# Kernel optimization log

Measured on AMD Instinct MI355X. Metric: run time of the kernel, lower is better.

Reference implementation:

```python
import jax, jax.numpy as jnp
import numpy as np

N, C, K, KEIG, B, NG, H = 32768, 128, 5, 128, 64, 512, 4
E = 524288
EPS = 1e-5


def setup_inputs() -> dict:
    key = jax.random.key(0)
    ks = iter(jax.random.split(key, 40))
    def nrm(shape, scale):
        return jax.random.normal(next(ks), shape, jnp.float32) * scale
    s = 1.0 / np.sqrt(C)
    return dict(
        x=nrm((N, C), 1.0),
        U=nrm((N, KEIG), 1.0 / np.sqrt(N)),
        Lambda=jax.random.uniform(next(ks), (KEIG,), jnp.float32, 0.0, 2.0),
        lambda_max=jnp.full((1,), 2.0, jnp.float32),
        w_spa1=nrm((C, C), s), b_spa1=jnp.zeros((C,), jnp.float32),
        w_spa2=nrm((C, C), s), b_spa2=jnp.zeros((C,), jnp.float32),
        w_spe1=nrm((C, C), s), b_spe1=jnp.zeros((C,), jnp.float32),
        w_spe2=nrm((C, C), s), b_spe2=jnp.zeros((C,), jnp.float32),
        cheb_w=nrm((K, C, C), s), cheb_b=jnp.zeros((C,), jnp.float32),
        gamma=jnp.ones((1,), jnp.float32),
        w_proj=nrm((C, C), s),
        w_qkv=nrm((C, 3 * C), s), b_qkv=jnp.zeros((3 * C,), jnp.float32),
        w_out=nrm((C, C), s), b_out=jnp.zeros((C,), jnp.float32),
        mlp_w1=nrm((C, 2 * C), s), mlp_b1=jnp.zeros((2 * C,), jnp.float32),
        mlp_w2=nrm((2 * C, C), 1.0 / np.sqrt(2 * C)), mlp_b2=jnp.zeros((C,), jnp.float32),
        bn1_w=jnp.ones((C,), jnp.float32), bn1_b=jnp.zeros((C,), jnp.float32),
        bn2_w=jnp.ones((C,), jnp.float32), bn2_b=jnp.zeros((C,), jnp.float32),
        bn3_w=jnp.ones((C,), jnp.float32), bn3_b=jnp.zeros((C,), jnp.float32),
        edge_index=jax.random.randint(next(ks), (2, E), 0, N, jnp.int64) if jax.config.jax_enable_x64 else jax.random.randint(next(ks), (2, E), 0, N, jnp.int32),
        batch=jnp.repeat(jnp.arange(B), NG),  # 64 graphs of 512 nodes each
    )


def _mlp2(h, w1, b1, w2, b2):
    return jnp.maximum(h @ w1 + b1, 0.0) @ w2 + b2


def _bn(h, w, b):
    # train-mode BatchNorm1d over node dim (biased variance), GPSConv default norm
    mu = h.mean(0)
    var = jnp.mean((h - mu) ** 2, 0)
    return (h - mu) * jax.lax.rsqrt(var + EPS) * w + b


def _cheb(x, src, dst, lam, Ws, bias):
    # L_hat = (2/lambda_max) * (I - D^{-1/2} A D^{-1/2}) - I ; sym normalization
    deg = jax.ops.segment_sum(jnp.ones_like(src, x.dtype), src, num_segments=N)
    dis = jnp.where(deg > 0, 1.0 / jnp.sqrt(deg), 0.0)
    w = dis[src] * dis[dst]  # [E]
    scale = 2.0 / lam
    def lhat(v):
        agg = jax.ops.segment_sum(w[:, None] * v[src], dst, num_segments=N)
        return (scale - 1.0) * v - scale * agg
    Tx0 = x
    out = Tx0 @ Ws[0]
    Tx1 = lhat(Tx0)
    out = out + Tx1 @ Ws[1]
    for k in range(2, K):
        Tx2 = 2.0 * lhat(Tx1) - Tx0
        out = out + Tx2 @ Ws[k]
        Tx0, Tx1 = Tx1, Tx2
    return out + bias


def _mha(xd, w_qkv, b_qkv, w_out, b_out):
    Bq, n, _ = xd.shape
    dh = C // H
    qkv = xd @ w_qkv + b_qkv  # [B,n,3C]
    q, k, v = jnp.split(qkv, 3, axis=-1)
    heads = lambda t: t.reshape(Bq, n, H, dh).transpose(0, 2, 1, 3)
    q, k, v = heads(q), heads(k), heads(v)
    a = jax.nn.softmax(jnp.einsum('bhqd,bhkd->bhqk', q, k) / np.sqrt(dh), axis=-1)
    o = jnp.einsum('bhqk,bhkd->bhqd', a, v).transpose(0, 2, 1, 3).reshape(Bq, n, C)
    return o @ w_out + b_out


def reference(x, U, Lambda, lambda_max,
              w_spa1, b_spa1, w_spa2, b_spa2,
              w_spe1, b_spe1, w_spe2, b_spe2,
              cheb_w, cheb_b, gamma, w_proj,
              w_qkv, b_qkv, w_out, b_out,
              mlp_w1, mlp_b1, mlp_w2, mlp_b2,
              bn1_w, bn1_b, bn2_w, bn2_b, bn3_w, bn3_b,
              edge_index, batch):
    src, dst = edge_index[0], edge_index[1]
    lam = lambda_max[0]
    # ---- SpectralLocalNN (GPSConv local conv branch) ----
    x_sp = _mlp2(x, w_spa1, b_spa1, w_spa2, b_spa2)
    out_local = _cheb(x_sp, src, dst, lam, cheb_w, cheb_b)
    x_spec = _mlp2(x, w_spe1, b_spe1, w_spe2, b_spe2)
    h_proj = x_spec @ w_proj
    s_lam = jnp.exp(-gamma[0] * Lambda ** 2)  # [k_eig]
    out_spectral = U @ (s_lam[:, None] * (U.T @ h_proj))
    h1 = _bn(out_local + out_spectral + x, bn1_w, bn1_b)
    # ---- global attention branch (equal-size graphs -> dense reshape) ----
    xd = x.reshape(B, NG, C)
    h2 = _mha(xd, w_qkv, b_qkv, w_out, b_out).reshape(N, C)
    h2 = _bn(h2 + x, bn2_w, bn2_b)
    # ---- combine + MLP ----
    out = h1 + h2
    out = out + _mlp2(out, mlp_w1, mlp_b1, mlp_w2, mlp_b2)
    return _bn(out, bn3_w, bn3_b)
```

## Files before the change

### kernel.cpp

```cpp
#include <hip/hip_runtime.h>

typedef short bf16x8 __attribute__((ext_vector_type(8)));
typedef short bf16x4 __attribute__((ext_vector_type(4)));
typedef float f32x4 __attribute__((ext_vector_type(4)));

#define DEVI __device__ __forceinline__

constexpr int N   = 32768;
constexpr int C   = 128;
constexpr int E   = 524288;
constexpr float EPSV = 1e-5f;
constexpr int UT_BLOCKS = 256;
constexpr int HB  = 128;
constexpr int EPB = E / HB;
constexpr float QSCALE = 0.17677669529663687f * 1.4426950408889634f;

DEVI float bf2f(ushort u){ return __uint_as_float(((uint)u) << 16); }
DEVI ushort f2bf(float f){
  uint u = __float_as_uint(f);
  return (ushort)((u + 0x7fffu + ((u >> 16) & 1u)) >> 16);
}
DEVI uint cvtpk(float lo, float hi){
  uint r;
  asm("v_cvt_pk_bf16_f32 %0, %1, %2" : "=v"(r) : "v"(lo), "v"(hi));
  return r;
}
DEVI float fexp2(float x){
  float r;
  asm("v_exp_f32 %0, %1" : "=v"(r) : "v"(x));
  return r;
}
DEVI float sane(float v){ if (!(v == v)) return 0.f; return fminf(fmaxf(v, -1e30f), 1e30f); }
DEVI bool mode_fp32(const uint* lmraw){ return (lmraw[0] & 0xffffu) == 0u; }

constexpr int CSZ[28] = {128,1,16384,128,16384,128,16384,128,16384,128,81920,128,
                         1,16384,49152,384,16384,128,32768,256,32768,128,
                         128,128,128,128,128,128};
constexpr int COF[28] = {0,128,192,16576,16704,33088,33216,49600,49728,66112,
                         66240,148160,148288,148352,164736,213888,214272,230656,
                         230784,263552,263808,296576,296704,296832,296960,297088,
                         297216,297344};
constexpr int CAN_SMALL_TOTAL = 297472;

constexpr int WT_SPA1 = 0;
constexpr int WT_SPA2 = 16384;
constexpr int WT_SPE1 = 32768;
constexpr int WT_SPE2 = 49152;
constexpr int WT_PROJ = 65536;
constexpr int WT_CHEB = 81920;
constexpr int WT_QKV  = 163840;
constexpr int WT_WOUT = 212992;
constexpr int WT_MLP1 = 229376;
constexpr int WT_MLP2 = 262144;
constexpr int WT_TOTAL = 294912;

struct CvtArgs { const void* src[28]; };

DEVI ushort cvt_elem(const void* p, int j, bool f32){
  return f32 ? f2bf(((const float*)p)[j]) : ((const ushort*)p)[j];
}

__global__ __launch_bounds__(256) void prep_all(CvtArgs a,
    const void* __restrict__ xs, const void* __restrict__ Us,
    ushort* __restrict__ canx, ushort* __restrict__ canu,
    ushort* __restrict__ cs, ushort* __restrict__ wt,
    int* __restrict__ zp, const uint* __restrict__ lmraw)
{
  bool f32 = mode_fp32(lmraw);
  int b = blockIdx.x, tid = threadIdx.x;
  if (b < 8192) {
    size_t e = ((size_t)b * 256 + tid) * 4;
    bool isU = e >= (size_t)N * C;
    size_t off = isU ? e - (size_t)N * C : e;
    const void* src = isU ? Us : xs;
    ushort* dst = isU ? canu : canx;
    ushort4 o;
    if (f32) {
      float4 v = *(const float4*)((const float*)src + off);
      o.x = f2bf(v.x); o.y = f2bf(v.y); o.z = f2bf(v.z); o.w = f2bf(v.w);
    } else {
      o = *(const ushort4*)((const ushort*)src + off);
    }
    *(ushort4*)(dst + off) = o;
  } else if (b < 9354) {
    int idx = (b - 8192) * 256 + tid;
    #pragma unroll 1
    for (int s = 0; s < 28; s++) {
      if (idx < CSZ[s]) { cs[COF[s] + idx] = cvt_elem(a.src[s], idx, f32); return; }
      idx -= CSZ[s];
    }
  } else if (b < 10506) {
    int i = (b - 9354) * 256 + tid;
    if (i < 81920) {
      int m = i >> 14, r = i & 16383; int k = r >> 7, n = r & 127;
      const void* src = m==0?a.src[2] : m==1?a.src[4] : m==2?a.src[6] : m==3?a.src[8] : a.src[13];
      wt[m*16384 + n*128 + k] = cvt_elem(src, r, f32);
    } else if (i < 163840) {
      int j = i - 81920; int m = j >> 14, r = j & 16383; int k = r >> 7, n = r & 127;
      wt[WT_CHEB + n*640 + m*128 + k] = cvt_elem(a.src[10], j, f32);
    } else if (i < 212992) {
      int j = i - 163840; int k = j / 384, n = j % 384;
      wt[WT_QKV + n*128 + k] = cvt_elem(a.src[14], j, f32);
    } else if (i < 229376) {
      int j = i - 212992; int k = j >> 7, n = j & 127;
      wt[WT_WOUT + n*128 + k] = cvt_elem(a.src[16], j, f32);
    } else if (i < 262144) {
      int j = i - 229376; int k = j >> 8, n = j & 255;
      wt[WT_MLP1 + n*128 + k] = cvt_elem(a.src[18], j, f32);
    } else if (i < WT_TOTAL) {
      int j = i - 262144; int k = j >> 7, n = j & 127;
      wt[WT_MLP2 + n*256 + k] = cvt_elem(a.src[20], j, f32);
    }
  } else {
    int i = (b - 10506) * 256 + tid;
    if (i < 6144) zp[i] = 0;
  }
}

__global__ __launch_bounds__(1024) void hist_lds(const int* __restrict__ ei,
    int* __restrict__ cei, ushort* __restrict__ part)
{
  __shared__ uint hist[N / 2];
  int t = threadIdx.x;
  int b = blockIdx.x;
  bool i64 = ((ei[1] | ei[3] | ei[5] | ei[7]) == 0);
  size_t j0 = (size_t)b * EPB;
  #pragma unroll
  for (int i = t; i < N / 2; i += 1024) hist[i] = 0u;
  __syncthreads();
  for (int k = t; k < EPB; k += 1024) {
    size_t j = j0 + k;
    int v = (i64 ? ei[2 * j] : ei[j]) & (N - 1);
    cei[j] = v;
    atomicAdd(&hist[v >> 1], 1u << ((v & 1) * 16));
  }
  __syncthreads();
  uint* po = (uint*)(part + (size_t)b * N);
  for (int i = t; i < N / 2; i += 1024) po[i] = hist[i];
}

__global__ __launch_bounds__(256) void reduce_cnt(const ushort* __restrict__ part,
    int* __restrict__ cdt, float* __restrict__ dis)
{
  int d = blockIdx.x * 256 + threadIdx.x;
  int s = 0, tt = 0;
  #pragma unroll 8
  for (int b = 0; b < HB; b++) s  += part[(size_t)b * N + d];
  #pragma unroll 8
  for (int b = 0; b < HB; b++) tt += part[(size_t)(HB + b) * N + d];
  cdt[d] = tt;
  dis[d] = s > 0 ? rsqrtf((float)s) : 0.f;
}

__global__ __launch_bounds__(1024) void scan_kernel(const int* __restrict__ cnt,
                                                    int* __restrict__ row_ptr)
{
  __shared__ int sums[1024];
  int t = threadIdx.x;
  int loc[32]; int s = 0;
  int base = t * 32;
  #pragma unroll
  for (int i = 0; i < 32; i++) { loc[i] = s; s += cnt[base + i]; }
  sums[t] = s;
  __syncthreads();
  for (int off = 1; off < 1024; off <<= 1) {
    int v = (t >= off) ? sums[t - off] : 0;
    __syncthreads();
    sums[t] += v;
    __syncthreads();
  }
  int pre = (t == 0) ? 0 : sums[t - 1];
  #pragma unroll
  for (int i = 0; i < 32; i++) row_ptr[base + i] = pre + loc[i];
}

__global__ __launch_bounds__(256) void off_kernel(const int* __restrict__ rp,
    const ushort* __restrict__ part, int* __restrict__ off2)
{
  int d = blockIdx.x * 256 + threadIdx.x;
  int run = rp[d];
  #pragma unroll 8
  for (int b = 0; b < HB; b++) {
    off2[(size_t)b * N + d] = run;
    run += part[(size_t)(HB + b) * N + d];
  }
}

__global__ __launch_bounds__(1024) void edge_scatter(const int* __restrict__ cei,
    const int* __restrict__ off2, const float* __restrict__ dis,
    int2* __restrict__ ep)
{
  __shared__ int base[N];
  int t = threadIdx.x;
  int b = blockIdx.x;
  for (int i = t; i < N; i += 1024) base[i] = off2[(size_t)b * N + i];
  __syncthreads();
  size_t e0 = (size_t)b * EPB;
  for (int k = t; k < EPB; k += 1024) {
    size_t e = e0 + k;
    int s = cei[e], d = cei[e + E];
    int slot = atomicAdd(&base[d], 1);
    int2 v; v.x = s; v.y = __float_as_int(dis[s] * dis[d]);
    ep[slot] = v;
  }
}

template<int K, int COLS, bool RELU, int OMODE, bool BIAS, bool RES, int ASTR, int OSTR, bool QSC, bool STATS>
__global__ __launch_bounds__(256) void gemm_lds(
    const ushort* __restrict__ A, const ushort* __restrict__ WT,
    const ushort* __restrict__ bias, const ushort* __restrict__ res,
    void* __restrict__ outp, float* __restrict__ gstats)
{
  constexpr int NSEG = COLS / 128;
  constexpr int NKC = K / 128;
  constexpr int BP = 136;
  __shared__ ushort Bs[128 * BP];
  __shared__ float ls[STATS ? 256 : 1];
  int tid = threadIdx.x;
  int lane = tid & 63, wave = tid >> 6;
  int quad = lane >> 4, l16 = lane & 15;
  int seg = (NSEG > 1) ? (blockIdx.x % NSEG) : 0;
  int rb  = (NSEG > 1) ? (blockIdx.x / NSEG) : blockIdx.x;
  int row0 = rb * 64 + wave * 16;
  const ushort* wseg = WT + (size_t)(seg * 128) * K;

  f32x4 acc[8];
  #pragma unroll
  for (int nt = 0; nt < 8; nt++) acc[nt] = (f32x4){0.f, 0.f, 0.f, 0.f};

  for (int kc = 0; kc < NKC; kc++) {
    if (kc) __syncthreads();
    #pragma unroll
    for (int i = tid; i < 2048; i += 256) {
      int col = i >> 4, ko = (i & 15) * 8;
      *(bf16x8*)&Bs[col * BP + ko] =
          *(const bf16x8*)(wseg + (size_t)col * K + kc * 128 + ko);
    }
    __syncthreads();
    bf16x8 a[4];
    const ushort* ap = A + (size_t)(row0 + l16) * ASTR + kc * 128 + quad * 8;
    #pragma unroll
    for (int kk = 0; kk < 4; kk++) a[kk] = *(const bf16x8*)(ap + kk * 32);
    #pragma unroll
    for (int kk = 0; kk < 4; kk++) {
      #pragma unroll
      for (int nt = 0; nt < 8; nt++) {
        bf16x8 b = *(const bf16x8*)(&Bs[(nt * 16 + l16) * BP + kk * 32 + quad * 8]);
        acc[nt] = __builtin_amdgcn_mfma_f32_16x16x32_bf16(a[kk], b, acc[nt], 0, 0, 0);
      }
    }
  }

  if (STATS) {
    if (tid < 256) ls[tid] = 0.f;
    __syncthreads();
  }

  #pragma unroll
  for (int nt = 0; nt < 8; nt++) {
    int col = seg * 128 + nt * 16 + l16;
    float bv = 0.f;
    if (BIAS) bv = bf2f(bias[col]);
    float cs_ = 0.f, cs2 = 0.f;
    #pragma unroll
    for (int r = 0; r < 4; r++) {
      int row = row0 + quad * 4 + r;
      size_t oi = (size_t)row * OSTR + col;
      float v = acc[nt][r] + bv;
      if (RES) v += bf2f(res[(size_t)row * COLS + col]);
      if (RELU) v = fmaxf(v, 0.f);
      if (QSC && col < 128) v *= QSCALE;
      float nv;
      if (OMODE == 0)      { ((ushort*)outp)[oi] = f2bf(v); nv = v; }
      else if (OMODE == 1) { ((float*)outp)[oi] = v; nv = v; }
      else                 { float* fo = (float*)outp + oi; nv = *fo + v; *fo = nv; }
      if (STATS) { float sv = sane(nv); cs_ += sv; cs2 += sv * sv; }
    }
    if (STATS) { atomicAdd(&ls[col], cs_); atomicAdd(&ls[128 + col], cs2); }
  }

  if (STATS) {
    __syncthreads();
    float* gs = gstats + (blockIdx.x & 7) * 256;
    if (tid < 128) {
      atomicAdd(&gs[tid], ls[tid]);
      atomicAdd(&gs[128 + tid], ls[128 + tid]);
    }
  }
}

__global__ __launch_bounds__(256) void gemm_qkv(
    const ushort* __restrict__ A, const ushort* __restrict__ WT,
    const ushort* __restrict__ bias, ushort* __restrict__ outp)
{
  constexpr int BP = 136;
  __shared__ ushort Bs[128 * BP];
  int tid = threadIdx.x;
  int lane = tid & 63, wave = tid >> 6;
  int quad = lane >> 4, l16 = lane & 15;
  int row0 = blockIdx.x * 64 + wave * 16;
  bf16x8 a[4];
  {
    const ushort* ap = A + (size_t)(row0 + l16) * 128 + quad * 8;
    #pragma unroll
    for (int kk = 0; kk < 4; kk++) a[kk] = *(const bf16x8*)(ap + kk * 32);
  }

  #pragma unroll 1
  for (int seg = 0; seg < 3; seg++) {
    if (seg) __syncthreads();
    for (int i = tid; i < 2048; i += 256) {
      int col = i >> 4, ko = (i & 15) * 8;
      *(bf16x8*)&Bs[col * BP + ko] =
          *(const bf16x8*)(WT + (size_t)(seg * 128 + col) * 128 + ko);
    }
    __syncthreads();
    f32x4 acc[8];
    #pragma unroll
    for (int nt = 0; nt < 8; nt++) acc[nt] = (f32x4){0.f, 0.f, 0.f, 0.f};
    #pragma unroll
    for (int kk = 0; kk < 4; kk++)
      #pragma unroll
      for (int nt = 0; nt < 8; nt++) {
        bf16x8 b = *(const bf16x8*)(&Bs[(nt * 16 + l16) * BP + kk * 32 + quad * 8]);
        acc[nt] = __builtin_amdgcn_mfma_f32_16x16x32_bf16(a[kk], b, acc[nt], 0, 0, 0);
      }
    #pragma unroll
    for (int nt = 0; nt < 8; nt++) {
      int col = seg * 128 + nt * 16 + l16;
      float bv = bf2f(bias[col]);
      #pragma unroll
      for (int r = 0; r < 4; r++) {
        float v = acc[nt][r] + bv;
        if (seg == 0) v *= QSCALE;
        outp[(size_t)(row0 + quad * 4 + r) * 384 + col] = f2bf(v);
      }
    }
  }
}

template<bool THIRD, int OSTR>
__global__ __launch_bounds__(256) void gemm_chain(
    const ushort* __restrict__ A,
    const ushort* __restrict__ W1, const ushort* __restrict__ B1,
    const ushort* __restrict__ W2, const ushort* __restrict__ B2,
    const ushort* __restrict__ W3,
    ushort* __restrict__ outp)
{
  constexpr int BP = 136;
  __shared__ ushort Bs[128 * BP];
  __shared__ ushort Ts[64 * BP];
  int tid = threadIdx.x;
  int lane = tid & 63, wave = tid >> 6;
  int quad = lane >> 4, l16 = lane & 15;
  int row0 = blockIdx.x * 64 + wave * 16;
  int lw = wave * 16;

  for (int i = tid; i < 2048; i += 256) {
    int col = i >> 4, ko = (i & 15) * 8;
    *(bf16x8*)&Bs[col * BP + ko] = *(const bf16x8*)(W1 + (size_t)col * 128 + ko);
  }
  __syncthreads();
  bf16x8 a[4];
  {
    const ushort* ap = A + (size_t)(row0 + l16) * 128 + quad * 8;
    #pragma unroll
    for (int kk = 0; kk < 4; kk++) a[kk] = *(const bf16x8*)(ap + kk * 32);
  }
  f32x4 acc[8];
  #pragma unroll
  for (int nt = 0; nt < 8; nt++) acc[nt] = (f32x4){0.f, 0.f, 0.f, 0.f};
  #pragma unroll
  for (int kk = 0; kk < 4; kk++)
    #pragma unroll
    for (int nt = 0; nt < 8; nt++) {
      bf16x8 b = *(const bf16x8*)(&Bs[(nt * 16 + l16) * BP + kk * 32 + quad * 8]);
      acc[nt] = __builtin_amdgcn_mfma_f32_16x16x32_bf16(a[kk], b, acc[nt], 0, 0, 0);
    }
  #pragma unroll
  for (int nt = 0; nt < 8; nt++) {
    int col = nt * 16 + l16;
    float bv = bf2f(B1[col]);
    #pragma unroll
    for (int r = 0; r < 4; r++)
      Ts[(lw + quad * 4 + r) * BP + col] = f2bf(fmaxf(acc[nt][r] + bv, 0.f));
  }
  __syncthreads();

  for (int i = tid; i < 2048; i += 256) {
    int col = i >> 4, ko = (i & 15) * 8;
    *(bf16x8*)&Bs[col * BP + ko] = *(const bf16x8*)(W2 + (size_t)col * 128 + ko);
  }
  #pragma unroll
  for (int kk = 0; kk < 4; kk++)
    a[kk] = *(const bf16x8*)(&Ts[(lw + l16) * BP + kk * 32 + quad * 8]);
  __syncthreads();
  #pragma unroll
  for (int nt = 0; nt < 8; nt++) acc[nt] = (f32x4){0.f, 0.f, 0.f, 0.f};
  #pragma unroll
  for (int kk = 0; kk < 4; kk++)
    #pragma unroll
    for (int nt = 0; nt < 8; nt++) {
      bf16x8 b = *(const bf16x8*)(&Bs[(nt * 16 + l16) * BP + kk * 32 + quad * 8]);
      acc[nt] = __builtin_amdgcn_mfma_f32_16x16x32_bf16(a[kk], b, acc[nt], 0, 0, 0);
    }

  if (!THIRD) {
    #pragma unroll
    for (int nt = 0; nt < 8; nt++) {
      int col = nt * 16 + l16;
      float bv = bf2f(B2[col]);
      #pragma unroll
      for (int r = 0; r < 4; r++)
        outp[(size_t)(row0 + quad * 4 + r) * OSTR + col] = f2bf(acc[nt][r] + bv);
    }
    return;
  }

  __syncthreads();
  #pragma unroll
  for (int nt = 0; nt < 8; nt++) {
    int col = nt * 16 + l16;
    float bv = bf2f(B2[col]);
    #pragma unroll
    for (int r = 0; r < 4; r++)
      Ts[(lw + quad * 4 + r) * BP + col] = f2bf(acc[nt][r] + bv);
  }
  __syncthreads();
  for (int i = tid; i < 2048; i += 256) {
    int col = i >> 4, ko = (i & 15) * 8;
    *(bf16x8*)&Bs[col * BP + ko] = *(const bf16x8*)(W3 + (size_t)col * 128 + ko);
  }
  #pragma unroll
  for (int kk = 0; kk < 4; kk++)
    a[kk] = *(const bf16x8*)(&Ts[(lw + l16) * BP + kk * 32 + quad * 8]);
  __syncthreads();
  #pragma unroll
  for (int nt = 0; nt < 8; nt++) acc[nt] = (f32x4){0.f, 0.f, 0.f, 0.f};
  #pragma unroll
  for (int kk = 0; kk < 4; kk++)
    #pragma unroll
    for (int nt = 0; nt < 8; nt++) {
      bf16x8 b = *(const bf16x8*)(&Bs[(nt * 16 + l16) * BP + kk * 32 + quad * 8]);
      acc[nt] = __builtin_amdgcn_mfma_f32_16x16x32_bf16(a[kk], b, acc[nt], 0, 0, 0);
    }
  #pragma unroll
  for (int nt = 0; nt < 8; nt++) {
    int col = nt * 16 + l16;
    #pragma unroll
    for (int r = 0; r < 4; r++)
      outp[(size_t)(row0 + quad * 4 + r) * OSTR + col] = f2bf(acc[nt][r]);
  }
}

__global__ __launch_bounds__(256) void gemm_mlp(
    const float* __restrict__ F1a, const float* __restrict__ F1b,
    const float* __restrict__ st1, const float* __restrict__ st2,
    const ushort* __restrict__ bw1, const ushort* __restrict__ bb1,
    const ushort* __restrict__ bw2, const ushort* __restrict__ bb2,
    const ushort* __restrict__ W1, const ushort* __restrict__ B1,
    const ushort* __restrict__ W2, const ushort* __restrict__ B2,
    float* __restrict__ outp, float* __restrict__ gstats)
{
  constexpr int BP = 136;
  constexpr int HP = 264;
  __shared__ ushort Bs[128 * BP];
  __shared__ ushort Hs[64 * HP];
  __shared__ float ls[256];
  __shared__ float kc1[128], oc1[128], kc2[128], oc2[128];
  int tid = threadIdx.x;
  int lane = tid & 63, wave = tid >> 6;
  int quad = lane >> 4, l16 = lane & 15;
  int row0 = blockIdx.x * 64 + wave * 16;
  int lw = wave * 16;

  if (tid < 128) {
    float s = 0.f, s2 = 0.f, t = 0.f, t2 = 0.f;
    #pragma unroll
    for (int rr = 0; rr < 8; rr++) {
      s  += st1[rr * 256 + tid];  s2 += st1[rr * 256 + 128 + tid];
      t  += st2[rr * 256 + tid];  t2 += st2[rr * 256 + 128 + tid];
    }
    float mu  = s * (1.f / 32768.f);
    float var = fmaxf(s2 * (1.f / 32768.f) - mu * mu, 0.f);
    float k = rsqrtf(var + EPSV) * bf2f(bw1[tid]);
    kc1[tid] = k; oc1[tid] = bf2f(bb1[tid]) - mu * k;
    mu  = t * (1.f / 32768.f);
    var = fmaxf(t2 * (1.f / 32768.f) - mu * mu, 0.f);
    k = rsqrtf(var + EPSV) * bf2f(bw2[tid]);
    kc2[tid] = k; oc2[tid] = bf2f(bb2[tid]) - mu * k;
  }
  __syncthreads();

  bf16x8 a[4];
  {
    int arow = row0 + l16;
    const float* pa = F1a + (size_t)arow * 128;
    const float* pb = F1b + (size_t)arow * 128;
    #pragma unroll
    for (int kk = 0; kk < 4; kk++) {
      int c0 = kk * 32 + quad * 8;
      float4 xa0 = *(const float4*)(pa + c0);
      float4 xa1 = *(const float4*)(pa + c0 + 4);
      float4 xb0 = *(const float4*)(pb + c0);
      float4 xb1 = *(const float4*)(pb + c0 + 4);
      float xa[8] = {xa0.x, xa0.y, xa0.z, xa0.w, xa1.x, xa1.y, xa1.z, xa1.w};
      float xb[8] = {xb0.x, xb0.y, xb0.z, xb0.w, xb1.x, xb1.y, xb1.z, xb1.w};
      bf16x8 frag;
      #pragma unroll
      for (int j = 0; j < 8; j++) {
        int c = c0 + j;
        float h1v = bf2f(f2bf(sane(xa[j]) * kc1[c] + oc1[c]));
        frag[j] = (short)f2bf(sane(xb[j]) * kc2[c] + oc2[c] + h1v);
      }
      a[kk] = frag;
    }
  }

  for (int seg = 0; seg < 2; seg++) {
    if (seg) __syncthreads();
    for (int i = tid; i < 2048; i += 256) {
      int col = i >> 4, ko = (i & 15) * 8;
      *(bf16x8*)&Bs[col * BP + ko] =
          *(const bf16x8*)(W1 + (size_t)(seg * 128 + col) * 128 + ko);
    }
    __syncthreads();
    f32x4 acc[8];
    #pragma unroll
    for (int nt = 0; nt < 8; nt++) acc[nt] = (f32x4){0.f, 0.f, 0.f, 0.f};
    #pragma unroll
    for (int kk = 0; kk < 4; kk++)
      #pragma unroll
      for (int nt = 0; nt < 8; nt++) {
        bf16x8 b = *(const bf16x8*)(&Bs[(nt * 16 + l16) * BP + kk * 32 + quad * 8]);
        acc[nt] = __builtin_amdgcn_mfma_f32_16x16x32_bf16(a[kk], b, acc[nt], 0, 0, 0);
      }
    #pragma unroll
    for (int nt = 0; nt < 8; nt++) {
      int col = seg * 128 + nt * 16 + l16;
      float bv = bf2f(B1[col]);
      #pragma unroll
      for (int r = 0; r < 4; r++)
        Hs[(lw + quad * 4 + r) * HP + col] = f2bf(fmaxf(acc[nt][r] + bv, 0.f));
    }
  }
  __syncthreads();
  if (tid < 256) ls[tid] = 0.f;

  f32x4 acc2[8];
  #pragma unroll
  for (int nt = 0; nt < 8; nt++) acc2[nt] = (f32x4){0.f, 0.f, 0.f, 0.f};
  for (int kc = 0; kc < 2; kc++) {
    if (kc) __syncthreads();
    for (int i = tid; i < 2048; i += 256) {
      int col = i >> 4, ko = (i & 15) * 8;
      *(bf16x8*)&Bs[col * BP + ko] =
          *(const bf16x8*)(W2 + (size_t)col * 256 + kc * 128 + ko);
    }
    bf16x8 a2[4];
    #pragma unroll
    for (int kk = 0; kk < 4; kk++)
      a2[kk] = *(const bf16x8*)(&Hs[(lw + l16) * HP + kc * 128 + kk * 32 + quad * 8]);
    __syncthreads();
    #pragma unroll
    for (int kk = 0; kk < 4; kk++)
      #pragma unroll
      for (int nt = 0; nt < 8; nt++) {
        bf16x8 b = *(const bf16x8*)(&Bs[(nt * 16 + l16) * BP + kk * 32 + quad * 8]);
        acc2[nt] = __builtin_amdgcn_mfma_f32_16x16x32_bf16(a2[kk], b, acc2[nt], 0, 0, 0);
      }
  }

  #pragma unroll
  for (int nt = 0; nt < 8; nt++) {
    int col = nt * 16 + l16;
    float bv = bf2f(B2[col]);
    float cs_ = 0.f, cs2 = 0.f;
    #pragma unroll
    for (int r = 0; r < 4; r++) {
      int row = row0 + quad * 4 + r;
      float xa = sane(F1a[(size_t)row * 128 + col]);
      float xb = sane(F1b[(size_t)row * 128 + col]);
      float h1v = bf2f(f2bf(xa * kc1[col] + oc1[col]));
      ushort cb = f2bf(xb * kc2[col] + oc2[col] + h1v);
      float v = acc2[nt][r] + bv + bf2f(cb);
      outp[(size_t)row * 128 + col] = v;
      float sv = sane(v); cs_ += sv; cs2 += sv * sv;
    }
    atomicAdd(&ls[col], cs_); atomicAdd(&ls[128 + col], cs2);
  }
  __syncthreads();
  float* gs = gstats + (blockIdx.x & 7) * 256;
  if (tid < 128) {
    atomicAdd(&gs[tid], ls[tid]);
    atomicAdd(&gs[128 + tid], ls[128 + tid]);
  }
}

__global__ __launch_bounds__(256) void spmm_cheb(
    const int* __restrict__ row_ptr, const int2* __restrict__ ep,
    const ushort* __restrict__ v,
    const ushort* __restrict__ txprev, ushort* __restrict__ txout,
    const ushort* __restrict__ lambda_max, int first, int str)
{
  int wave = threadIdx.x >> 6, lane = threadIdx.x & 63;
  int sub = lane >> 4, l16 = lane & 15;
  int d = blockIdx.x * 4 + wave;
  float lm = bf2f(lambda_max[0]);
  float scale = 2.f / lm;
  if (!(scale == scale) || fabsf(scale) > 1e6f) scale = 1.f;
  int beg = row_ptr[d];
  int end = (d == N - 1) ? E : row_ptr[d + 1];
  float acc[8] = {0.f,0.f,0.f,0.f,0.f,0.f,0.f,0.f};
  int j0 = beg + sub;
  int2 eA = ep[j0 < end ? j0 : 0];
  int2 eB = ep[(j0 + 4) < end ? (j0 + 4) : 0];
  bf16x8 vA = *(const bf16x8*)(v + (size_t)(eA.x & (N - 1)) * str + l16 * 8);
  for (int jb = beg; jb < end; jb += 4) {
    int jc = jb + 8 + sub;
    int2 eC = ep[jc < end ? jc : 0];
    bf16x8 vB = *(const bf16x8*)(v + (size_t)(eB.x & (N - 1)) * str + l16 * 8);
    bool ok = (jb + sub) < end;
    float w = ok ? __int_as_float(eA.y) : 0.f;
    #pragma unroll
    for (int i = 0; i < 8; i++) acc[i] += w * bf2f((ushort)vA[i]);
    eA = eB; eB = eC; vA = vB;
  }
  #pragma unroll
  for (int i = 0; i < 8; i++) {
    acc[i] += __shfl_xor(acc[i], 16);
    acc[i] += __shfl_xor(acc[i], 32);
  }
  if (sub == 0) {
    bf16x8 vd = *(const bf16x8*)(v + (size_t)d * str + l16 * 8);
    bf16x8 tp;
    if (!first) tp = *(const bf16x8*)(txprev + (size_t)d * str + l16 * 8);
    bf16x8 ov;
    #pragma unroll
    for (int i = 0; i < 8; i++) {
      float r = (scale - 1.f) * bf2f((ushort)vd[i]) - scale * acc[i];
      if (!first) r = 2.f * r - bf2f((ushort)tp[i]);
      ov[i] = (short)f2bf(r);
    }
    *(bf16x8*)(txout + (size_t)d * str + l16 * 8) = ov;
  }
}

__global__ __launch_bounds__(256) void ut_mfma(const ushort* __restrict__ U,
    const ushort* __restrict__ hp, float* __restrict__ parts)
{
  constexpr int RP = 40;
  __shared__ ushort Ut[128 * RP];
  __shared__ ushort Ht[128 * RP];
  int t = threadIdx.x;
  int lane = t & 63, wave = t >> 6;
  int quad = lane >> 4, l16 = lane & 15;

  f32x4 acc[2][8];
  #pragma unroll
  for (int a = 0; a < 2; a++)
    #pragma unroll
    for (int ct = 0; ct < 8; ct++) acc[a][ct] = (f32x4){0.f, 0.f, 0.f, 0.f};

  for (int ch = 0; ch < 4; ch++) {
    int n0 = blockIdx.x * 128 + ch * 32;
    __syncthreads();
    for (int i = t; i < 2048; i += 256) {
      int r2 = i >> 7, c = i & 127;
      uint u0 = U [(size_t)(n0 + r2 * 2) * 128 + c];
      uint u1 = U [(size_t)(n0 + r2 * 2 + 1) * 128 + c];
      *(uint*)&Ut[c * RP + r2 * 2] = (u0 & 0xffffu) | (u1 << 16);
      uint h0 = hp[(size_t)(n0 + r2 * 2) * 128 + c];
      uint h1 = hp[(size_t)(n0 + r2 * 2 + 1) * 128 + c];
      *(uint*)&Ht[c * RP + r2 * 2] = (h0 & 0xffffu) | (h1 << 16);
    }
    __syncthreads();
    bf16x8 bfr[8];
    #pragma unroll
    for (int ct = 0; ct < 8; ct++)
      bfr[ct] = *(const bf16x8*)(&Ht[(ct * 16 + l16) * RP + quad * 8]);
    #pragma unroll
    for (int a = 0; a < 2; a++) {
      int kt = wave * 2 + a;
      bf16x8 af = *(const bf16x8*)(&Ut[(kt * 16 + l16) * RP + quad * 8]);
      #pragma unroll
      for (int ct = 0; ct < 8; ct++)
        acc[a][ct] = __builtin_amdgcn_mfma_f32_16x16x32_bf16(af, bfr[ct], acc[a][ct], 0, 0, 0);
    }
  }

  float* po = parts + (size_t)blockIdx.x * 16384;
  #pragma unroll
  for (int a = 0; a < 2; a++) {
    int kt = wave * 2 + a;
    #pragma unroll
    for (int ct = 0; ct < 8; ct++)
      #pragma unroll
      for (int r = 0; r < 4; r++)
        po[(kt * 16 + quad * 4 + r) * 128 + ct * 16 + l16] = acc[a][ct][r];
  }
}

__global__ __launch_bounds__(256) void reduce_mt(const float* __restrict__ parts,
    const ushort* __restrict__ Lambda, const ushort* __restrict__ gamma,
    ushort* __restrict__ MT)
{
  int e = blockIdx.x * 256 + threadIdx.x;
  int keig = e >> 7, c = e & 127;
  float s = 0.f;
  for (int p = 0; p < UT_BLOCKS; p++) s += parts[(size_t)p * 16384 + e];
  float g = bf2f(gamma[0]);
  float lam = bf2f(Lambda[keig]);
  float sl = __expf(-g * lam * lam);
  MT[c * 128 + keig] = f2bf(sl * s);
}

__global__ __launch_bounds__(256) void bn_apply(const float* __restrict__ h,
    const float* __restrict__ st, const ushort* __restrict__ gw,
    const ushort* __restrict__ gb, const ushort* __restrict__ add,
    void* __restrict__ out, const uint* __restrict__ lmraw, int final_out)
{
  __shared__ float sk[128], sb[128];
  int tid = threadIdx.x;
  if (tid < 128) {
    float s = 0.f, s2 = 0.f;
    #pragma unroll
    for (int rr = 0; rr < 8; rr++) {
      s  += st[rr * 256 + tid];
      s2 += st[rr * 256 + 128 + tid];
    }
    float mu  = s * (1.f / 32768.f);
    float var = fmaxf(s2 * (1.f / 32768.f) - mu * mu, 0.f);
    float k = rsqrtf(var + EPSV) * bf2f(gw[tid]);
    sk[tid] = k;
    sb[tid] = bf2f(gb[tid]) - mu * k;
  }
  __syncthreads();
  size_t e = ((size_t)blockIdx.x * 256 + tid) * 4;
  int c0 = (int)(e & 127);
  float4 hv = *(const float4*)(h + e);
  float xv[4] = {sane(hv.x), sane(hv.y), sane(hv.z), sane(hv.w)};
  float addv[4] = {0.f, 0.f, 0.f, 0.f};
  if (add) {
    ushort4 av = *(const ushort4*)(add + e);
    addv[0] = bf2f(av.x); addv[1] = bf2f(av.y);
    addv[2] = bf2f(av.z); addv[3] = bf2f(av.w);
  }
  float r[4];
  #pragma unroll
  for (int j = 0; j < 4; j++) {
    int c = c0 + j;
    r[j] = xv[j] * sk[c] + sb[c] + addv[j];
  }
  if (final_out && mode_fp32(lmraw)) {
    float4 o4; o4.x = r[0]; o4.y = r[1]; o4.z = r[2]; o4.w = r[3];
    *(float4*)((float*)out + e) = o4;
  } else {
    ushort4 o;
    o.x = f2bf(r[0]); o.y = f2bf(r[1]); o.z = f2bf(r[2]); o.w = f2bf(r[3]);
    *(ushort4*)((ushort*)out + e) = o;
  }
}

__global__ __launch_bounds__(512) void attn_mfma(const ushort* __restrict__ qkv,
                                                 ushort* __restrict__ attn)
{
  constexpr int VP = 516;
  constexpr int KP = 40;
  __shared__ ushort Kt[512 * KP];
  __shared__ ushort Vt[32 * VP];
  int b = blockIdx.x;
  int g = b >> 3, hh = (b >> 1) & 3, half = b & 1;
  int lane = threadIdx.x & 63, wave = threadIdx.x >> 6;
  int quad = lane >> 4, l16 = lane & 15;
  const ushort* base = qkv + (size_t)g * 512 * 384;

  for (int i = threadIdx.x; i < 512 * 4; i += 512) {
    int key = i >> 2, c8 = (i & 3) * 8;
    *(bf16x8*)&Kt[key * KP + c8] =
        *(const bf16x8*)(base + (size_t)key * 384 + 128 + hh * 32 + c8);
  }
  for (int i = threadIdx.x; i < 256 * 8; i += 512) {
    int kp = i >> 3, d4 = (i & 7) * 4;
    const ushort* va = base + (size_t)(2 * kp) * 384 + 256 + hh * 32 + d4;
    ushort4 a = *(const ushort4*)va;
    ushort4 c = *(const ushort4*)(va + 384);
    *(uint*)&Vt[(d4 + 0) * VP + 2 * kp] = (uint)a.x | ((uint)c.x << 16);
    *(uint*)&Vt[(d4 + 1) * VP + 2 * kp] = (uint)a.y | ((uint)c.y << 16);
    *(uint*)&Vt[(d4 + 2) * VP + 2 * kp] = (uint)a.z | ((uint)c.z << 16);
    *(uint*)&Vt[(d4 + 3) * VP + 2 * kp] = (uint)a.w | ((uint)c.w << 16);
  }
  __syncthreads();

  int q0 = half * 256 + wave * 32;
  bf16x8 qf[2];
  #pragma unroll
  for (int i = 0; i < 2; i++)
    qf[i] = *(const bf16x8*)(base + (size_t)(q0 + i * 16 + l16) * 384 + hh * 32 + quad * 8);

  f32x4 O[2][2];
  #pragma unroll
  for (int dt = 0; dt < 2; dt++)
    #pragma unroll
    for (int i = 0; i < 2; i++) O[dt][i] = (f32x4){0.f, 0.f, 0.f, 0.f};
  float lsum[2] = {0.f, 0.f};

  union PU { uint u[4]; bf16x8 v; };
  union VU { uint2 a[2]; bf16x8 v; };

  for (int kt2 = 0; kt2 < 16; kt2++) {
    int k0 = kt2 * 32;
    bf16x8 kfA = *(const bf16x8*)&Kt[(k0 + l16) * KP + quad * 8];
    bf16x8 kfB = *(const bf16x8*)&Kt[(k0 + 16 + l16) * KP + quad * 8];
    PU pw[2];
    #pragma unroll
    for (int i = 0; i < 2; i++) {
      f32x4 sA = __builtin_amdgcn_mfma_f32_16x16x32_bf16(kfA, qf[i], (f32x4){0.f,0.f,0.f,0.f}, 0, 0, 0);
      f32x4 sB = __builtin_amdgcn_mfma_f32_16x16x32_bf16(kfB, qf[i], (f32x4){0.f,0.f,0.f,0.f}, 0, 0, 0);
      float p0 = fexp2(fminf(sA[0], 86.5f));
      float p1 = fexp2(fminf(sA[1], 86.5f));
      float p2 = fexp2(fminf(sA[2], 86.5f));
      float p3 = fexp2(fminf(sA[3], 86.5f));
      float p4 = fexp2(fminf(sB[0], 86.5f));
      float p5 = fexp2(fminf(sB[1], 86.5f));
      float p6 = fexp2(fminf(sB[2], 86.5f));
      float p7 = fexp2(fminf(sB[3], 86.5f));
      lsum[i] += ((p0 + p1) + (p2 + p3)) + ((p4 + p5) + (p6 + p7));
      pw[i].u[0] = cvtpk(p0, p1); pw[i].u[1] = cvtpk(p2, p3);
      pw[i].u[2] = cvtpk(p4, p5); pw[i].u[3] = cvtpk(p6, p7);
    }
    #pragma unroll
    for (int dt = 0; dt < 2; dt++) {
      int drow = (dt * 16 + l16) * VP;
      VU vu;
      vu.a[0] = *(const uint2*)&Vt[drow + k0 + quad * 4];
      vu.a[1] = *(const uint2*)&Vt[drow + k0 + 16 + quad * 4];
      #pragma unroll
      for (int i = 0; i < 2; i++)
        O[dt][i] = __builtin_amdgcn_mfma_f32_16x16x32_bf16(vu.v, pw[i].v, O[dt][i], 0, 0, 0);
    }
  }

  #pragma unroll
  for (int i = 0; i < 2; i++) {
    float l = lsum[i];
    l += __shfl_xor(l, 16);
    l += __shfl_xor(l, 32);
    lsum[i] = 1.f / l;
  }

  #pragma unroll
  for (int i = 0; i < 2; i++) {
    size_t node = (size_t)g * 512 + q0 + i * 16 + l16;
    #pragma unroll
    for (int dt = 0; dt < 2; dt++) {
      uint2 o;
      o.x = cvtpk(O[dt][i][0] * lsum[i], O[dt][i][1] * lsum[i]);
      o.y = cvtpk(O[dt][i][2] * lsum[i], O[dt][i][3] * lsum[i]);
      *(uint2*)(attn + node * 128 + hh * 32 + dt * 16 + quad * 4) = o;
    }
  }
}

constexpr size_t KB = 1024;
constexpr size_t MB = 1048576;
constexpr size_t OFF_WT    = 0;
constexpr size_t OFF_CDT   = 576 * KB;
constexpr size_t OFF_RP    = 704 * KB;
constexpr size_t OFF_DIS   = 832 * KB;
constexpr size_t OFF_MT    = 960 * KB;
constexpr size_t OFF_STATS = 1024 * KB;
constexpr size_t OFF_CEI   = 6  * MB;
constexpr size_t OFF_EP    = 10 * MB;
constexpr size_t OFF_CANX  = 14 * MB;
constexpr size_t OFF_CANU  = 22 * MB;
constexpr size_t OFF_CANS  = 30 * MB;
constexpr size_t OFF_F1    = 31 * MB;
constexpr size_t OFF_HPROJ = 39 * MB;
constexpr size_t OFF_TBIG  = 47 * MB;
constexpr size_t OFF_PARTH = OFF_TBIG;
constexpr size_t OFF_OFF2  = OFF_TBIG + 16 * MB;
constexpr size_t OFF_F1B   = 71 * MB;
constexpr size_t OFF_PARTS = 87 * MB;

extern "C" void kernel_launch(void* const* d_in, const int* in_sizes, int n_in,
                              void* d_out, int out_size, void* d_ws, size_t ws_size,
                              hipStream_t stream) {
  (void)in_sizes; (void)n_in; (void)out_size; (void)ws_size;
  const uint* lmraw = (const uint*)d_in[3];
  const int*  ei    = (const int*)d_in[30];

  char* W = (char*)d_ws;
  ushort* wt    = (ushort*)(W + OFF_WT);
  int*    cdt   = (int*)(W + OFF_CDT);
  int*    rp    = (int*)(W + OFF_RP);
  float*  dis   = (float*)(W + OFF_DIS);
  ushort* MT    = (ushort*)(W + OFF_MT);
  float*  stats = (float*)(W + OFF_STATS);
  int*    cei   = (int*)(W + OFF_CEI);
  int2*   ep    = (int2*)(W + OFF_EP);
  ushort* part  = (ushort*)(W + OFF_PARTH);
  int*    off2  = (int*)(W + OFF_OFF2);
  ushort* canx  = (ushort*)(W + OFF_CANX);
  ushort* canu  = (ushort*)(W + OFF_CANU);
  ushort* cs    = (ushort*)(W + OFF_CANS);
  float*  F1    = (float*)(W + OFF_F1);
  float*  F1B   = (float*)(W + OFF_F1B);
  ushort* hproj = (ushort*)(W + OFF_HPROJ);
  ushort* Tbig  = (ushort*)(W + OFF_TBIG);
  ushort* qkvb  = (ushort*)(W + OFF_TBIG);
  float*  parts = (float*)(W + OFF_PARTS);
  ushort* attnb = (ushort*)(W + OFF_PARTS);

  const ushort* cLambda = cs + COF[0];
  const ushort* cLmx    = cs + COF[1];
  const ushort* cBspa1  = cs + COF[3];
  const ushort* cBspa2  = cs + COF[5];
  const ushort* cBspe1  = cs + COF[7];
  const ushort* cBspe2  = cs + COF[9];
  const ushort* cChebB  = cs + COF[11];
  const ushort* cGam    = cs + COF[12];
  const ushort* cBqkv   = cs + COF[15];
  const ushort* cBout   = cs + COF[17];
  const ushort* cMb1    = cs + COF[19];
  const ushort* cMb2    = cs + COF[21];
  const ushort* cBn1w   = cs + COF[22];
  const ushort* cBn1b   = cs + COF[23];
  const ushort* cBn2w   = cs + COF[24];
  const ushort* cBn2b   = cs + COF[25];
  const ushort* cBn3w   = cs + COF[26];
  const ushort* cBn3b   = cs + COF[27];

  const ushort* NUL = nullptr;
  float* NULF = nullptr;

  CvtArgs ca;
  ca.src[0]  = d_in[2];  ca.src[1]  = d_in[3];  ca.src[2]  = d_in[4];
  ca.src[3]  = d_in[5];  ca.src[4]  = d_in[6];  ca.src[5]  = d_in[7];
  ca.src[6]  = d_in[8];  ca.src[7]  = d_in[9];  ca.src[8]  = d_in[10];
  ca.src[9]  = d_in[11]; ca.src[10] = d_in[12]; ca.src[11] = d_in[13];
  ca.src[12] = d_in[14]; ca.src[13] = d_in[15]; ca.src[14] = d_in[16];
  ca.src[15] = d_in[17]; ca.src[16] = d_in[18]; ca.src[17] = d_in[19];
  ca.src[18] = d_in[20]; ca.src[19] = d_in[21]; ca.src[20] = d_in[22];
  ca.src[21] = d_in[23]; ca.src[22] = d_in[24]; ca.src[23] = d_in[25];
  ca.src[24] = d_in[26]; ca.src[25] = d_in[27]; ca.src[26] = d_in[28];
  ca.src[27] = d_in[29];
  prep_all<<<10530, 256, 0, stream>>>(ca, d_in[0], d_in[1], canx, canu, cs, wt,
                                      (int*)(W + OFF_STATS), lmraw);

  hist_lds<<<2 * HB, 1024, 0, stream>>>(ei, cei, part);
  reduce_cnt<<<N / 256, 256, 0, stream>>>(part, cdt, dis);
  scan_kernel<<<1, 1024, 0, stream>>>(cdt, rp);
  off_kernel<<<N / 256, 256, 0, stream>>>(rp, part, off2);
  edge_scatter<<<HB, 1024, 0, stream>>>(cei, off2, dis, ep);

  dim3 g1(512), bb(256);
  gemm_chain<false, 640><<<g1, bb, 0, stream>>>(canx, wt + WT_SPA1, cBspa1,
      wt + WT_SPA2, cBspa2, NUL, Tbig);
  gemm_chain<true, 128><<<g1, bb, 0, stream>>>(canx, wt + WT_SPE1, cBspe1,
      wt + WT_SPE2, cBspe2, wt + WT_PROJ, hproj);

  ut_mfma<<<UT_BLOCKS, 256, 0, stream>>>(canu, hproj, parts);
  reduce_mt<<<64, 256, 0, stream>>>(parts, cLambda, cGam, MT);

  spmm_cheb<<<N / 4, 256, 0, stream>>>(rp, ep, Tbig,       NUL,        Tbig + 128, cLmx, 1, 640);
  spmm_cheb<<<N / 4, 256, 0, stream>>>(rp, ep, Tbig + 128, Tbig,       Tbig + 256, cLmx, 0, 640);
  spmm_cheb<<<N / 4, 256, 0, stream>>>(rp, ep, Tbig + 256, Tbig + 128, Tbig + 384, cLmx, 0, 640);
  spmm_cheb<<<N / 4, 256, 0, stream>>>(rp, ep, Tbig + 384, Tbig + 256, Tbig + 512, cLmx, 0, 640);
  gemm_lds<640,128,false,1,true ,false,640,128,false,false><<<g1, bb, 0, stream>>>(Tbig, wt + WT_CHEB, cChebB, NUL, F1, NULF);

  gemm_lds<128,128,false,2,false,true ,128,128,false,true ><<<g1, bb, 0, stream>>>(canu, MT, NUL, canx, F1, stats);

  gemm_qkv<<<g1, bb, 0, stream>>>(canx, wt + WT_QKV, cBqkv, qkvb);
  attn_mfma<<<512, 512, 0, stream>>>(qkvb, attnb);
  gemm_lds<128,128,false,1,true ,true ,128,128,false,true ><<<g1, bb, 0, stream>>>(attnb, wt + WT_WOUT, cBout, canx, F1B, stats + 2048);

  gemm_mlp<<<g1, bb, 0, stream>>>(F1, F1B, stats, stats + 2048,
      cBn1w, cBn1b, cBn2w, cBn2b,
      wt + WT_MLP1, cMb1, wt + WT_MLP2, cMb2, F1, stats + 4096);
  bn_apply<<<(N * C) / 1024, 256, 0, stream>>>(F1, stats + 4096, cBn3w, cBn3b, NUL, d_out, lmraw, 1);
}
```

Measured before the change: 470.1 us.

## Fuse Chebyshev GEMM with spectral U·MT GEMM and unroll SpMM gather loop

Replaces two GEMM launches (Chebyshev weight GEMM writing F1, then the spectral U@MT GEMM accumulating into F1 with residual and BN stats) with one kernel that accumulates both K-chunks in registers and writes once with bias, residual and stats. This removes an fp32 F1 write and read-modify-write pass plus a launch. Separately, the SpMM edge loop is changed from a software-pipelined 4-edge stride to issuing 4 independent gathers per 16-edge iteration to raise memory-level parallelism, at the cost of more registers and wasted lanes on low-degree rows.

```diff
diff --git a/kernel.cpp b/kernel.cpp
--- a/kernel.cpp
+++ b/kernel.cpp
@@ -289,6 +289,74 @@
   }
 }
 
+__global__ __launch_bounds__(256) void gemm_cheb_mt(
+    const ushort* __restrict__ Tb, const ushort* __restrict__ Wc,
+    const ushort* __restrict__ chebB,
+    const ushort* __restrict__ canu, const ushort* __restrict__ MT,
+    const ushort* __restrict__ canx,
+    float* __restrict__ outp, float* __restrict__ gstats)
+{
+  constexpr int BP = 136;
+  __shared__ ushort Bs[128 * BP];
+  __shared__ float ls[256];
+  int tid = threadIdx.x;
+  int lane = tid & 63, wave = tid >> 6;
+  int quad = lane >> 4, l16 = lane & 15;
+  int row0 = blockIdx.x * 64 + wave * 16;
+
+  f32x4 acc[8];
+  #pragma unroll
+  for (int nt = 0; nt < 8; nt++) acc[nt] = (f32x4){0.f, 0.f, 0.f, 0.f};
+
+  for (int kc = 0; kc < 6; kc++) {
+    if (kc) __syncthreads();
+    bool mt = (kc == 5);
+    for (int i = tid; i < 2048; i += 256) {
+      int col = i >> 4, ko = (i & 15) * 8;
+      *(bf16x8*)&Bs[col * BP + ko] = mt
+          ? *(const bf16x8*)(MT + (size_t)col * 128 + ko)
+          : *(const bf16x8*)(Wc + (size_t)col * 640 + kc * 128 + ko);
+    }
+    __syncthreads();
+    bf16x8 a[4];
+    const ushort* ap = mt ? canu + (size_t)(row0 + l16) * 128 + quad * 8
+                          : Tb   + (size_t)(row0 + l16) * 640 + kc * 128 + quad * 8;
+    #pragma unroll
+    for (int kk = 0; kk < 4; kk++) a[kk] = *(const bf16x8*)(ap + kk * 32);
+    #pragma unroll
+    for (int kk = 0; kk < 4; kk++)
+      #pragma unroll
+      for (int nt = 0; nt < 8; nt++) {
+        bf16x8 b = *(const bf16x8*)(&Bs[(nt * 16 + l16) * BP + kk * 32 + quad * 8]);
+        acc[nt] = __builtin_amdgcn_mfma_f32_16x16x32_bf16(a[kk], b, acc[nt], 0, 0, 0);
+      }
+  }
+
+  if (tid < 256) ls[tid] = 0.f;
+  __syncthreads();
+
+  #pragma unroll
+  for (int nt = 0; nt < 8; nt++) {
+    int col = nt * 16 + l16;
+    float bv = bf2f(chebB[col]);
+    float cs_ = 0.f, cs2 = 0.f;
+    #pragma unroll
+    for (int r = 0; r < 4; r++) {
+      int row = row0 + quad * 4 + r;
+      float v = acc[nt][r] + bv + bf2f(canx[(size_t)row * 128 + col]);
+      outp[(size_t)row * 128 + col] = v;
+      float sv = sane(v); cs_ += sv; cs2 += sv * sv;
+    }
+    atomicAdd(&ls[col], cs_); atomicAdd(&ls[128 + col], cs2);
+  }
+  __syncthreads();
+  float* gs = gstats + (blockIdx.x & 7) * 256;
+  if (tid < 128) {
+    atomicAdd(&gs[tid], ls[tid]);
+    atomicAdd(&gs[128 + tid], ls[128 + tid]);
+  }
+}
+
 __global__ __launch_bounds__(256) void gemm_qkv(
     const ushort* __restrict__ A, const ushort* __restrict__ WT,
     const ushort* __restrict__ bias, ushort* __restrict__ outp)
@@ -612,19 +680,28 @@
   int beg = row_ptr[d];
   int end = (d == N - 1) ? E : row_ptr[d + 1];
   float acc[8] = {0.f,0.f,0.f,0.f,0.f,0.f,0.f,0.f};
-  int j0 = beg + sub;
-  int2 eA = ep[j0 < end ? j0 : 0];
-  int2 eB = ep[(j0 + 4) < end ? (j0 + 4) : 0];
-  bf16x8 vA = *(const bf16x8*)(v + (size_t)(eA.x & (N - 1)) * str + l16 * 8);
-  for (int jb = beg; jb < end; jb += 4) {
-    int jc = jb + 8 + sub;
-    int2 eC = ep[jc < end ? jc : 0];
-    bf16x8 vB = *(const bf16x8*)(v + (size_t)(eB.x & (N - 1)) * str + l16 * 8);
-    bool ok = (jb + sub) < end;
-    float w = ok ? __int_as_float(eA.y) : 0.f;
-    #pragma unroll
-    for (int i = 0; i < 8; i++) acc[i] += w * bf2f((ushort)vA[i]);
-    eA = eB; eB = eC; vA = vB;
+  for (int jb = beg; jb < end; jb += 16) {
+    int j0 = jb + sub, j1 = jb + 4 + sub, j2 = jb + 8 + sub, j3 = jb + 12 + sub;
+    int2 e0 = ep[j0 < end ? j0 : 0];
+    int2 e1 = ep[j1 < end ? j1 : 0];
+    int2 e2 = ep[j2 < end ? j2 : 0];
+    int2 e3 = ep[j3 < end ? j3 : 0];
+    bf16x8 v0 = *(const bf16x8*)(v + (size_t)(e0.x & (N - 1)) * str + l16 * 8);
+    bf16x8 v1 = *(const bf16x8*)(v + (size_t)(e1.x & (N - 1)) * str + l16 * 8);
+    bf16x8 v2 = *(const bf16x8*)(v + (size_t)(e2.x & (N - 1)) * str + l16 * 8);
+    bf16x8 v3 = *(const bf16x8*)(v + (size_t)(e3.x & (N - 1)) * str + l16 * 8);
+    float w0 = j0 < end ? __int_as_float(e0.y) : 0.f;
+    float w1 = j1 < end ? __int_as_float(e1.y) : 0.f;
+    float w2 = j2 < end ? __int_as_float(e2.y) : 0.f;
+    float w3 = j3 < end ? __int_as_float(e3.y) : 0.f;
+    #pragma unroll
+    for (int i = 0; i < 8; i++) acc[i] += w0 * bf2f((ushort)v0[i]);
+    #pragma unroll
+    for (int i = 0; i < 8; i++) acc[i] += w1 * bf2f((ushort)v1[i]);
+    #pragma unroll
+    for (int i = 0; i < 8; i++) acc[i] += w2 * bf2f((ushort)v2[i]);
+    #pragma unroll
+    for (int i = 0; i < 8; i++) acc[i] += w3 * bf2f((ushort)v3[i]);
   }
   #pragma unroll
   for (int i = 0; i < 8; i++) {
@@ -967,9 +1044,9 @@
   spmm_cheb<<<N / 4, 256, 0, stream>>>(rp, ep, Tbig + 128, Tbig,       Tbig + 256, cLmx, 0, 640);
   spmm_cheb<<<N / 4, 256, 0, stream>>>(rp, ep, Tbig + 256, Tbig + 128, Tbig + 384, cLmx, 0, 640);
   spmm_cheb<<<N / 4, 256, 0, stream>>>(rp, ep, Tbig + 384, Tbig + 256, Tbig + 512, cLmx, 0, 640);
-  gemm_lds<640,128,false,1,true ,false,640,128,false,false><<<g1, bb, 0, stream>>>(Tbig, wt + WT_CHEB, cChebB, NUL, F1, NULF);
-
-  gemm_lds<128,128,false,2,false,true ,128,128,false,true ><<<g1, bb, 0, stream>>>(canu, MT, NUL, canx, F1, stats);
+
+  gemm_cheb_mt<<<g1, bb, 0, stream>>>(Tbig, wt + WT_CHEB, cChebB, canu, MT, canx,
+                                      F1, stats);
 
   gemm_qkv<<<g1, bb, 0, stream>>>(canx, wt + WT_QKV, cBqkv, qkvb);
   attn_mfma<<<512, 512, 0, stream>>>(qkvb, attnb);
```

Result: no change. 469.6 us (-0.1%).
